# Optimization experiments

Hardware: AMD Instinct MI355X
Metric: run time of the kernel (lower is better)

Reference implementation:

```python
import jax, jax.numpy as jnp
import numpy as np

C = 1024   # n_embd = dim_att = dim_k = dim_v
H = 16     # n_head
K = 64     # k_head_size
V = 64     # v_head_size
DF = 2048  # dim_ffn = (2*C)//32*32
B = 4
T = 1024
N_LAYER = 24
LAYER_ID = 12


def setup_inputs() -> dict:
    key = jax.random.key(0)
    ks = jax.random.split(key, 8)
    r01 = LAYER_ID / (N_LAYER - 1)
    r10 = 1.0 - LAYER_ID / N_LAYER
    ddd = (jnp.arange(C, dtype=jnp.float32) / C)[None, None, :]
    maa_x = 1.0 - ddd ** r10
    maa_k = 1.0 - ddd ** r10
    maa_v = 1.0 - (ddd ** r10 + 0.3 * r01)
    maa_r = 1.0 - ddd ** (0.5 * r10)
    n = jnp.arange(C, dtype=jnp.float32)
    zigzag = ((jnp.arange(C) + 1) % 3 - 1).astype(jnp.float32) * 0.1
    u = (r01 * (1.0 - n / (C - 1)) + zigzag).reshape(H, K)
    # LoRA mats: torch init is zeros / uniform(-0.01,0.01); use small uniform for both
    # so the token-shift LoRA path is actually exercised.
    w1 = jax.random.uniform(ks[0], (C, 96), minval=-0.01, maxval=0.01)
    w2 = jax.random.uniform(ks[1], (3, 32, C), minval=-0.01, maxval=0.01)
    s = 0.02
    Wr = jax.random.normal(ks[2], (C, C)) * s
    Wk = jax.random.normal(ks[3], (C, C)) * s
    Wvg = jax.random.normal(ks[4], (C, 2 * (C + DF))) * s
    Wo = jax.random.normal(ks[5], (C + DF, C)) * s
    ln_g = jnp.ones((C,), jnp.float32)
    ln_b = jnp.zeros((C,), jnp.float32)
    x = jax.random.normal(ks[6], (B, T, C), dtype=jnp.float32)
    return dict(x=x, maa_x=maa_x, maa_k=maa_k, maa_v=maa_v, maa_r=maa_r,
                w1=w1, w2=w2, u=u, Wr=Wr, Wk=Wk, Wvg=Wvg, Wo=Wo,
                ln_g=ln_g, ln_b=ln_b)


def _wkv6(r, k, v, e, u):
    # r,k,e: (B,T,H,K); v: (B,T,H,V); u: (H,K). Decayed linear-attention scan.
    rt = r.transpose(1, 0, 2, 3)
    kt = k.transpose(1, 0, 2, 3)
    vt = v.transpose(1, 0, 2, 3)
    et = e.transpose(1, 0, 2, 3)

    def step(S, inp):  # S: (B,H,K,V)
        r_t, k_t, v_t, e_t = inp
        kv = k_t[..., :, None] * v_t[..., None, :]           # (B,H,K,V)
        out = jnp.einsum('bhk,bhkv->bhv', r_t, S + u[None, :, :, None] * kv)
        return S * e_t[..., :, None] + kv, out

    S0 = jnp.zeros((r.shape[0], u.shape[0], u.shape[1], v.shape[-1]), r.dtype)
    _, o = jax.lax.scan(step, S0, (rt, kt, vt, et))
    return o.transpose(1, 0, 2, 3)  # (B,T,H,V)


def reference(x, maa_x, maa_k, maa_v, maa_r, w1, w2, u, Wr, Wk, Wvg, Wo, ln_g, ln_b):
    Bx, Tx, Cx = x.shape
    # time_shift: ZeroPad2d((0,0,1,-1)) -> shift right by 1 along T with zero pad
    xs = jnp.concatenate([jnp.zeros_like(x[:, :1]), x[:, :-1]], axis=1)
    xx = xs - x
    xxx = x + xx * maa_x
    m = jnp.tanh(xxx @ w1).reshape(Bx, Tx, 3, -1)        # (B,T,3,32)
    m = jnp.einsum('btld,ldc->lbtc', m, w2)              # (3,B,T,C)
    mk, mv, mr = m[0], m[1], m[2]
    xk = x + xx * (maa_k + mk)
    xv = x + xx * (maa_v + mv)
    xr = x + xx * (maa_r + mr)
    r = xr @ Wr
    w = xk @ Wk
    e = jnp.exp(-jnp.exp(w))   # per-channel decay used by the WKV kernel
    k = 1.0 - e                # k = 1 - exp(-exp(w))
    vg = xv @ Wvg
    vffn, gate = jnp.split(vg, 2, axis=-1)
    vffn = vffn * jax.nn.silu(gate)
    v, ffn = vffn[..., :Cx], vffn[..., Cx:]
    o = _wkv6(r.reshape(Bx, Tx, H, K), k.reshape(Bx, Tx, H, K),
              v.reshape(Bx, Tx, H, V), e.reshape(Bx, Tx, H, K), u)
    o = o.reshape(Bx, Tx, Cx)
    mu = o.mean(-1, keepdims=True)
    var = o.var(-1, keepdims=True)
    o = (o - mu) / jnp.sqrt(var + 1e-5) * ln_g + ln_b
    return jnp.concatenate([o, ffn], axis=-1) @ Wo
```

## Files before the change

kernel.cpp:

```cpp
#include <hip/hip_runtime.h>
#include <hip/hip_bf16.h>
#include <math.h>

#define Bn 4
#define Tn 1024
#define Cn 1024
#define Hn 16
#define Kn 64
#define DFn 2048
#define NCn 16
#define Ln 64

typedef __bf16 bf16x8 __attribute__((ext_vector_type(8)));
typedef float f32x4 __attribute__((ext_vector_type(4)));

#define GLD(dst, src) \
  __builtin_amdgcn_global_load_lds((__attribute__((address_space(1))) const void*)(src), \
                                   (__attribute__((address_space(3))) void*)(dst), 16, 0, 0)

__device__ __forceinline__ float rdlane(float v, int l) {
  return __int_as_float(__builtin_amdgcn_readlane(__float_as_int(v), l));
}

__device__ __forceinline__ unsigned short bfbits(float f) {
  union { __hip_bfloat16 h; unsigned short u; } cv;
  cv.h = __float2bfloat16(f);
  return cv.u;
}

__global__ __launch_bounds__(256) void k_prep(const float* __restrict__ x,
                                              const float* __restrict__ maa_x,
                                              float* __restrict__ xx,
                                              __hip_bfloat16* __restrict__ xxx16) {
  int idx = blockIdx.x * 256 + threadIdx.x;
  int c4 = idx & 255;
  int bt = idx >> 8;
  int t = bt & (Tn - 1);
  const float4* x4 = (const float4*)x;
  float4 xv = x4[idx];
  float4 xp;
  if (t > 0) xp = x4[idx - 256];
  else { xp.x = 0.f; xp.y = 0.f; xp.z = 0.f; xp.w = 0.f; }
  float4 d;
  d.x = xp.x - xv.x; d.y = xp.y - xv.y; d.z = xp.z - xv.z; d.w = xp.w - xv.w;
  float4 m = ((const float4*)maa_x)[c4];
  ushort4 o;
  o.x = bfbits(fmaf(d.x, m.x, xv.x));
  o.y = bfbits(fmaf(d.y, m.y, xv.y));
  o.z = bfbits(fmaf(d.z, m.z, xv.z));
  o.w = bfbits(fmaf(d.w, m.w, xv.w));
  ((float4*)xx)[idx] = d;
  ((ushort4*)xxx16)[idx] = o;
}

__global__ __launch_bounds__(256) void k_mix1_16(const __hip_bfloat16* __restrict__ A,
                                                 const __hip_bfloat16* __restrict__ Bt,
                                                 __hip_bfloat16* __restrict__ m1) {
  const int K = 1024;
  __shared__ __align__(16) __hip_bfloat16 Al[128 * 32];
  __shared__ __align__(16) __hip_bfloat16 Bl[96 * 32];
  const int tid = threadIdx.x;
  const int wid = tid >> 6, lane = tid & 63;
  const int wr = wid >> 1, wc = wid & 1;
  const int row0 = blockIdx.x * 128;
  const char* gsrc[4];
  char* ldst[4];
  bool act[4];
  #pragma unroll
  for (int i = 0; i < 4; ++i) {
    const int s = i * 4 + wid;
    act[i] = (s < 14);
    const int ss = act[i] ? s : 0;
    if (ss < 8) {
      const int r = ss * 16 + (lane >> 2);
      gsrc[i] = (const char*)(A + (size_t)(row0 + r) * K) + (lane & 3) * 16;
      ldst[i] = (char*)&Al[0] + ss * 1024;
    } else {
      const int r = (ss - 8) * 16 + (lane >> 2);
      gsrc[i] = (const char*)(Bt + (size_t)r * K) + (lane & 3) * 16;
      ldst[i] = (char*)&Bl[0] + (ss - 8) * 1024;
    }
  }
  f32x4 acc[4][3];
  #pragma unroll
  for (int i = 0; i < 4; ++i)
    #pragma unroll
    for (int j = 0; j < 3; ++j)
      acc[i][j] = (f32x4){0.f, 0.f, 0.f, 0.f};
  const int g = lane >> 4, m = lane & 15;
  for (int k0 = 0; k0 < K; k0 += 32) {
    #pragma unroll
    for (int i = 0; i < 4; ++i) if (act[i]) GLD(ldst[i], gsrc[i]);
    #pragma unroll
    for (int i = 0; i < 4; ++i) gsrc[i] += 64;
    __syncthreads();
    bf16x8 af[4], bfr[3];
    #pragma unroll
    for (int i = 0; i < 4; ++i)
      af[i] = *(const bf16x8*)&Al[(wr * 64 + i * 16 + m) * 32 + g * 8];
    #pragma unroll
    for (int j = 0; j < 3; ++j)
      bfr[j] = *(const bf16x8*)&Bl[(wc * 48 + j * 16 + m) * 32 + g * 8];
    #pragma unroll
    for (int i = 0; i < 4; ++i)
      #pragma unroll
      for (int j = 0; j < 3; ++j)
        acc[i][j] = __builtin_amdgcn_mfma_f32_16x16x32_bf16(af[i], bfr[j], acc[i][j], 0, 0, 0);
    __syncthreads();
  }
  #pragma unroll
  for (int i = 0; i < 4; ++i) {
    const int grow = row0 + wr * 64 + i * 16 + g * 4;
    #pragma unroll
    for (int j = 0; j < 3; ++j) {
      const int gcol = wc * 48 + j * 16 + m;
      #pragma unroll
      for (int e = 0; e < 4; ++e)
        m1[(size_t)(grow + e) * 96 + gcol] = __float2bfloat16(tanhf(acc[i][j][e]));
    }
  }
}

__global__ __launch_bounds__(256) void k_mix2_16(const __hip_bfloat16* __restrict__ m1,
                                                 const __hip_bfloat16* __restrict__ w2t,
                                                 const float* __restrict__ x,
                                                 const float* __restrict__ xx,
                                                 const float* __restrict__ maa_k,
                                                 const float* __restrict__ maa_v,
                                                 const float* __restrict__ maa_r,
                                                 __hip_bfloat16* __restrict__ xk,
                                                 __hip_bfloat16* __restrict__ xv,
                                                 __hip_bfloat16* __restrict__ xr) {
  __shared__ __align__(16) __hip_bfloat16 Al[128 * 96];
  __shared__ __align__(16) __hip_bfloat16 Bl[3 * 64 * 32];
  const int tid = threadIdx.x;
  const int wid = tid >> 6, lane = tid & 63;
  const int wr = wid >> 1, wc = wid & 1;
  const int row0 = blockIdx.y * 128, col0 = blockIdx.x * 64;
  {
    const char* abase = (const char*)(m1 + (size_t)row0 * 96) + lane * 16;
    #pragma unroll
    for (int i = 0; i < 6; ++i) {
      const int s = wid + i * 4;
      GLD((char*)&Al[0] + s * 1024, abase + s * 1024);
    }
  }
  {
    const char* bbase = (const char*)w2t + (size_t)col0 * 64 + lane * 16;
    #pragma unroll
    for (int i = 0; i < 3; ++i) {
      const int s = wid + i * 4;
      const int l = s >> 2, q = s & 3;
      GLD((char*)&Bl[0] + s * 1024, bbase + (size_t)l * 65536 + q * 1024);
    }
  }
  __syncthreads();
  const int g = lane >> 4, m = lane & 15;
  f32x4 a0[4][2], a1[4][2], a2[4][2];
  #pragma unroll
  for (int i = 0; i < 4; ++i)
    #pragma unroll
    for (int j = 0; j < 2; ++j) {
      a0[i][j] = (f32x4){0.f,0.f,0.f,0.f};
      a1[i][j] = (f32x4){0.f,0.f,0.f,0.f};
      a2[i][j] = (f32x4){0.f,0.f,0.f,0.f};
    }
  #pragma unroll
  for (int l = 0; l < 3; ++l) {
    bf16x8 af[4], bfj[2];
    #pragma unroll
    for (int i = 0; i < 4; ++i)
      af[i] = *(const bf16x8*)&Al[(wr * 64 + i * 16 + m) * 96 + l * 32 + g * 8];
    #pragma unroll
    for (int j = 0; j < 2; ++j)
      bfj[j] = *(const bf16x8*)&Bl[(l * 64 + wc * 32 + j * 16 + m) * 32 + g * 8];
    #pragma unroll
    for (int i = 0; i < 4; ++i)
      #pragma unroll
      for (int j = 0; j < 2; ++j) {
        if (l == 0) a0[i][j] = __builtin_amdgcn_mfma_f32_16x16x32_bf16(af[i], bfj[j], a0[i][j], 0, 0, 0);
        if (l == 1) a1[i][j] = __builtin_amdgcn_mfma_f32_16x16x32_bf16(af[i], bfj[j], a1[i][j], 0, 0, 0);
        if (l == 2) a2[i][j] = __builtin_amdgcn_mfma_f32_16x16x32_bf16(af[i], bfj[j], a2[i][j], 0, 0, 0);
      }
  }
  #pragma unroll
  for (int i = 0; i < 4; ++i) {
    const int grow = row0 + wr * 64 + i * 16 + g * 4;
    #pragma unroll
    for (int j = 0; j < 2; ++j) {
      const int gcol = col0 + wc * 32 + j * 16 + m;
      const float mk_ = maa_k[gcol], mv_ = maa_v[gcol], mr_ = maa_r[gcol];
      #pragma unroll
      for (int e = 0; e < 4; ++e) {
        const size_t off = (size_t)(grow + e) * 1024 + gcol;
        const float xval = x[off], xxv = xx[off];
        xk[off] = __float2bfloat16(fmaf(xxv, mk_ + a0[i][j][e], xval));
        xv[off] = __float2bfloat16(fmaf(xxv, mv_ + a1[i][j][e], xval));
        xr[off] = __float2bfloat16(fmaf(xxv, mr_ + a2[i][j][e], xval));
      }
    }
  }
}

__global__ __launch_bounds__(256) void k_cvt_t(const float* __restrict__ W,
                                               __hip_bfloat16* __restrict__ Wt,
                                               int K, int N) {
  __shared__ float tile[32][33];
  int n0 = blockIdx.x * 32, k0 = blockIdx.y * 32;
  int tid = threadIdx.x;
  int c = tid & 31, r = tid >> 5;
  #pragma unroll
  for (int i = 0; i < 4; ++i)
    tile[r + i * 8][c] = W[(size_t)(k0 + r + i * 8) * N + n0 + c];
  __syncthreads();
  #pragma unroll
  for (int i = 0; i < 4; ++i)
    Wt[(size_t)(n0 + r + i * 8) * K + k0 + c] = __float2bfloat16(tile[c][r + i * 8]);
}

template <int FN, int EPI>
__global__ __launch_bounds__(256) void k_gemm16(const __hip_bfloat16* __restrict__ A,
                                                const __hip_bfloat16* __restrict__ Bt,
                                                float* __restrict__ C,
                                                const int K, const int N) {
  constexpr int BN = FN * 32;
  constexpr int NISS = 8 + BN / 16;
  constexpr int PW = NISS / 4;
  __shared__ __align__(16) __hip_bfloat16 Al[128 * 32];
  __shared__ __align__(16) __hip_bfloat16 Bl[BN * 32];
  const int tid = threadIdx.x;
  const int wid = tid >> 6, lane = tid & 63;
  const int wr = wid >> 1, wc = wid & 1;
  const int row0 = blockIdx.y * 128, col0 = blockIdx.x * BN;
  const char* gsrc[PW];
  char* ldst[PW];
  #pragma unroll
  for (int i = 0; i < PW; ++i) {
    const int s = wid + i * 4;
    if (s < 8) {
      const int r = s * 16 + (lane >> 2);
      gsrc[i] = (const char*)(A + (size_t)(row0 + r) * K) + (lane & 3) * 16;
      ldst[i] = (char*)&Al[0] + s * 1024;
    } else {
      const int r = (s - 8) * 16 + (lane >> 2);
      gsrc[i] = (const char*)(Bt + (size_t)(col0 + r) * K) + (lane & 3) * 16;
      ldst[i] = (char*)&Bl[0] + (s - 8) * 1024;
    }
  }
  f32x4 acc[4][FN];
  #pragma unroll
  for (int i = 0; i < 4; ++i)
    #pragma unroll
    for (int j = 0; j < FN; ++j)
      acc[i][j] = (f32x4){0.f, 0.f, 0.f, 0.f};
  const int g = lane >> 4, m = lane & 15;
  for (int k0 = 0; k0 < K; k0 += 32) {
    #pragma unroll
    for (int i = 0; i < PW; ++i) GLD(ldst[i], gsrc[i]);
    #pragma unroll
    for (int i = 0; i < PW; ++i) gsrc[i] += 64;
    __syncthreads();
    bf16x8 af[4], bfr[FN];
    #pragma unroll
    for (int i = 0; i < 4; ++i)
      af[i] = *(const bf16x8*)&Al[(wr * 64 + i * 16 + m) * 32 + g * 8];
    #pragma unroll
    for (int j = 0; j < FN; ++j)
      bfr[j] = *(const bf16x8*)&Bl[(wc * (BN / 2) + j * 16 + m) * 32 + g * 8];
    #pragma unroll
    for (int i = 0; i < 4; ++i)
      #pragma unroll
      for (int j = 0; j < FN; ++j)
        acc[i][j] = __builtin_amdgcn_mfma_f32_16x16x32_bf16(af[i], bfr[j], acc[i][j], 0, 0, 0);
    __syncthreads();
  }
  #pragma unroll
  for (int i = 0; i < 4; ++i) {
    const int grow = row0 + wr * 64 + i * 16 + g * 4;
    #pragma unroll
    for (int j = 0; j < FN; ++j) {
      const int gcol = col0 + wc * (BN / 2) + j * 16 + m;
      #pragma unroll
      for (int e = 0; e < 4; ++e) {
        float val = acc[i][j][e];
        if (EPI == 1) val = expf(-expf(val));
        C[(size_t)(grow + e) * N + gcol] = val;
      }
    }
  }
}

__global__ __launch_bounds__(256) void k_gemm_vg16(const __hip_bfloat16* __restrict__ A,
                                                   const __hip_bfloat16* __restrict__ Bt,
                                                   float* __restrict__ v,
                                                   __hip_bfloat16* __restrict__ ffn) {
  const int K = 1024;
  __shared__ __align__(16) __hip_bfloat16 Al[128 * 32];
  __shared__ __align__(16) __hip_bfloat16 B1l[64 * 32];
  __shared__ __align__(16) __hip_bfloat16 B2l[64 * 32];
  const int tid = threadIdx.x;
  const int wid = tid >> 6, lane = tid & 63;
  const int wr = wid >> 1, wc = wid & 1;
  const int row0 = blockIdx.y * 128, col0 = blockIdx.x * 64;
  const char* gsrc[4];
  char* ldst[4];
  #pragma unroll
  for (int i = 0; i < 4; ++i) {
    const int s = wid + i * 4;
    if (s < 8) {
      const int r = s * 16 + (lane >> 2);
      gsrc[i] = (const char*)(A + (size_t)(row0 + r) * K) + (lane & 3) * 16;
      ldst[i] = (char*)&Al[0] + s * 1024;
    } else if (s < 12) {
      const int r = col0 + (s - 8) * 16 + (lane >> 2);
      gsrc[i] = (const char*)(Bt + (size_t)r * K) + (lane & 3) * 16;
      ldst[i] = (char*)&B1l[0] + (s - 8) * 1024;
    } else {
      const int r = 3072 + col0 + (s - 12) * 16 + (lane >> 2);
      gsrc[i] = (const char*)(Bt + (size_t)r * K) + (lane & 3) * 16;
      ldst[i] = (char*)&B2l[0] + (s - 12) * 1024;
    }
  }
  f32x4 a1[4][2], a2[4][2];
  #pragma unroll
  for (int i = 0; i < 4; ++i)
    #pragma unroll
    for (int j = 0; j < 2; ++j) {
      a1[i][j] = (f32x4){0.f, 0.f, 0.f, 0.f};
      a2[i][j] = (f32x4){0.f, 0.f, 0.f, 0.f};
    }
  const int g = lane >> 4, m = lane & 15;
  for (int k0 = 0; k0 < K; k0 += 32) {
    #pragma unroll
    for (int i = 0; i < 4; ++i) GLD(ldst[i], gsrc[i]);
    #pragma unroll
    for (int i = 0; i < 4; ++i) gsrc[i] += 64;
    __syncthreads();
    bf16x8 af[4], b1f[2], b2f[2];
    #pragma unroll
    for (int i = 0; i < 4; ++i)
      af[i] = *(const bf16x8*)&Al[(wr * 64 + i * 16 + m) * 32 + g * 8];
    #pragma unroll
    for (int j = 0; j < 2; ++j) {
      b1f[j] = *(const bf16x8*)&B1l[(wc * 32 + j * 16 + m) * 32 + g * 8];
      b2f[j] = *(const bf16x8*)&B2l[(wc * 32 + j * 16 + m) * 32 + g * 8];
    }
    #pragma unroll
    for (int i = 0; i < 4; ++i)
      #pragma unroll
      for (int j = 0; j < 2; ++j) {
        a1[i][j] = __builtin_amdgcn_mfma_f32_16x16x32_bf16(af[i], b1f[j], a1[i][j], 0, 0, 0);
        a2[i][j] = __builtin_amdgcn_mfma_f32_16x16x32_bf16(af[i], b2f[j], a2[i][j], 0, 0, 0);
      }
    __syncthreads();
  }
  const bool to_v = (col0 < 1024);
  #pragma unroll
  for (int i = 0; i < 4; ++i) {
    const int grow = row0 + wr * 64 + i * 16 + g * 4;
    #pragma unroll
    for (int j = 0; j < 2; ++j) {
      const int gcol = col0 + wc * 32 + j * 16 + m;
      #pragma unroll
      for (int e = 0; e < 4; ++e) {
        float gate = a2[i][j][e];
        float val = a1[i][j][e] * (gate / (1.f + expf(-gate)));
        if (to_v) v[(size_t)(grow + e) * 1024 + gcol] = val;
        else ffn[(size_t)(grow + e) * 2048 + (gcol - 1024)] = __float2bfloat16(val);
      }
    }
  }
}

__global__ __launch_bounds__(256) void k_gemm_wo16(const __hip_bfloat16* __restrict__ A1,
                                                   const __hip_bfloat16* __restrict__ A2,
                                                   const __hip_bfloat16* __restrict__ Bt,
                                                   float* __restrict__ C) {
  const int Kt = 3072;
  __shared__ __align__(16) __hip_bfloat16 Al[128 * 32];
  __shared__ __align__(16) __hip_bfloat16 Bl[64 * 32];
  const int tid = threadIdx.x;
  const int wid = tid >> 6, lane = tid & 63;
  const int wr = wid >> 1, wc = wid & 1;
  const int row0 = blockIdx.y * 128, col0 = blockIdx.x * 64;
  const char* gsrc[3];
  char* ldst[3];
  #pragma unroll
  for (int i = 0; i < 3; ++i) {
    const int s = wid + i * 4;
    if (s < 8) {
      const int r = s * 16 + (lane >> 2);
      gsrc[i] = (const char*)(A1 + (size_t)(row0 + r) * 1024) + (lane & 3) * 16;
      ldst[i] = (char*)&Al[0] + s * 1024;
    } else {
      const int r = col0 + (s - 8) * 16 + (lane >> 2);
      gsrc[i] = (const char*)(Bt + (size_t)r * Kt) + (lane & 3) * 16;
      ldst[i] = (char*)&Bl[0] + (s - 8) * 1024;
    }
  }
  f32x4 acc[4][2];
  #pragma unroll
  for (int i = 0; i < 4; ++i)
    #pragma unroll
    for (int j = 0; j < 2; ++j)
      acc[i][j] = (f32x4){0.f, 0.f, 0.f, 0.f};
  const int g = lane >> 4, m = lane & 15;

  #define WO_STEP() do {                                                          \
    _Pragma("unroll")                                                             \
    for (int i = 0; i < 3; ++i) GLD(ldst[i], gsrc[i]);                            \
    _Pragma("unroll")                                                             \
    for (int i = 0; i < 3; ++i) gsrc[i] += 64;                                    \
    __syncthreads();                                                              \
    bf16x8 af[4], bfr[2];                                                         \
    _Pragma("unroll")                                                             \
    for (int i = 0; i < 4; ++i)                                                   \
      af[i] = *(const bf16x8*)&Al[(wr * 64 + i * 16 + m) * 32 + g * 8];           \
    _Pragma("unroll")                                                             \
    for (int j = 0; j < 2; ++j)                                                   \
      bfr[j] = *(const bf16x8*)&Bl[(wc * 32 + j * 16 + m) * 32 + g * 8];          \
    _Pragma("unroll")                                                             \
    for (int i = 0; i < 4; ++i)                                                   \
      _Pragma("unroll")                                                           \
      for (int j = 0; j < 2; ++j)                                                 \
        acc[i][j] = __builtin_amdgcn_mfma_f32_16x16x32_bf16(af[i], bfr[j],        \
                                                            acc[i][j], 0, 0, 0); \
    __syncthreads();                                                              \
  } while (0)

  for (int k0 = 0; k0 < 1024; k0 += 32) WO_STEP();
  #pragma unroll
  for (int i = 0; i < 3; ++i) {
    const int s = wid + i * 4;
    if (s < 8) {
      const int r = s * 16 + (lane >> 2);
      gsrc[i] = (const char*)(A2 + (size_t)(row0 + r) * 2048) + (lane & 3) * 16;
    }
  }
  for (int k0 = 0; k0 < 2048; k0 += 32) WO_STEP();
  #undef WO_STEP

  #pragma unroll
  for (int i = 0; i < 4; ++i) {
    const int grow = row0 + wr * 64 + i * 16 + g * 4;
    #pragma unroll
    for (int j = 0; j < 2; ++j) {
      const int gcol = col0 + wc * 32 + j * 16 + m;
      #pragma unroll
      for (int e = 0; e < 4; ++e)
        C[(size_t)(grow + e) * 1024 + gcol] = acc[i][j][e];
    }
  }
}

__global__ __launch_bounds__(256) void k_wkv1(const float* __restrict__ r,
                                              const float* __restrict__ e,
                                              const float* __restrict__ v,
                                              const float* __restrict__ u,
                                              float* __restrict__ o,
                                              float* __restrict__ Dcum,
                                              float* __restrict__ Dtot,
                                              float* __restrict__ Inc) {
  int blk = blockIdx.x;
  int c = blk & (NCn - 1);
  int bh = blk >> 4;
  int b = bh >> 4, h = bh & 15;
  int tid = threadIdx.x, wave = tid >> 6, lane = tid & 63;
  size_t base = (size_t)b * Tn * Cn + (size_t)h * 64 + (size_t)c * Ln * Cn;
  int jbase = wave * 16 + (lane & 15);
  float uv = u[h * 64 + jbase];
  float st[16];
  #pragma unroll
  for (int i = 0; i < 16; ++i) st[i] = 0.f;
  float cum = 1.f;
  __shared__ float yp[4][64];
  for (int t = 0; t < Ln; ++t) {
    size_t off = base + (size_t)t * Cn;
    float rv = r[off + jbase];
    float ev = e[off + jbase];
    float vv = v[off + lane];
    if (lane < 16) Dcum[off + jbase] = cum;
    cum *= ev;
    float y = 0.f;
    #pragma unroll
    for (int jj = 0; jj < 16; ++jj) {
      float rj = rdlane(rv, jj);
      float ej = rdlane(ev, jj);
      float uj = rdlane(uv, jj);
      float kv = (1.f - ej) * vv;
      y = fmaf(rj, fmaf(uj, kv, st[jj]), y);
      st[jj] = fmaf(st[jj], ej, kv);
    }
    yp[wave][lane] = y;
    __syncthreads();
    if (wave == 0)
      o[off + lane] = yp[0][lane] + yp[1][lane] + yp[2][lane] + yp[3][lane];
    __syncthreads();
  }
  size_t sbase = ((size_t)bh * NCn + c) * 4096;
  #pragma unroll
  for (int jj = 0; jj < 16; ++jj)
    Inc[sbase + (size_t)(wave * 16 + jj) * 64 + lane] = st[jj];
  if (lane < 16)
    Dtot[((size_t)bh * NCn + c) * 64 + jbase] = cum;
}

__global__ __launch_bounds__(256) void k_wkv2(float* __restrict__ S,
                                              const float* __restrict__ Dtot) {
  int bh = blockIdx.x;
  int tid = threadIdx.x;
  float4 s[4];
  #pragma unroll
  for (int j = 0; j < 4; ++j) { s[j].x = 0.f; s[j].y = 0.f; s[j].z = 0.f; s[j].w = 0.f; }
  size_t sb = (size_t)bh * NCn * 4096;
  for (int c = 0; c < NCn; ++c) {
    float4* entry = (float4*)(S + sb + (size_t)c * 4096);
    const float* dt = Dtot + ((size_t)bh * NCn + c) * 64;
    #pragma unroll
    for (int j = 0; j < 4; ++j) {
      int idx4 = tid + j * 256;
      int k = idx4 >> 4;
      float d = dt[k];
      float4 inc = entry[idx4];
      float4 cur = s[j];
      entry[idx4] = cur;
      s[j].x = fmaf(cur.x, d, inc.x);
      s[j].y = fmaf(cur.y, d, inc.y);
      s[j].z = fmaf(cur.z, d, inc.z);
      s[j].w = fmaf(cur.w, d, inc.w);
    }
  }
}

__global__ __launch_bounds__(256) void k_wkv3(const float* __restrict__ r,
                                              const float* __restrict__ Dcum,
                                              const float* __restrict__ S,
                                              float* __restrict__ o) {
  int blk = blockIdx.x;
  int c = blk & (NCn - 1);
  if (c == 0) return;
  int bh = blk >> 4;
  int b = bh >> 4, h = bh & 15;
  int tid = threadIdx.x, wave = tid >> 6, lane = tid & 63;
  const float* Sg = S + ((size_t)bh * NCn + c) * 4096;
  float sreg[64];
  #pragma unroll
  for (int k = 0; k < 64; ++k) sreg[k] = Sg[k * 64 + lane];
  size_t base = (size_t)b * Tn * Cn + (size_t)h * 64 + (size_t)c * Ln * Cn;
  for (int ti = 0; ti < 16; ++ti) {
    int t = wave * 16 + ti;
    size_t off = base + (size_t)t * Cn;
    float rd = r[off + lane] * Dcum[off + lane];
    float y = 0.f;
    #pragma unroll
    for (int k = 0; k < 64; ++k)
      y = fmaf(rdlane(rd, k), sreg[k], y);
    o[off + lane] += y;
  }
}

__global__ __launch_bounds__(256) void k_ln(const float* __restrict__ o,
                                            const float* __restrict__ g,
                                            const float* __restrict__ bta,
                                            __hip_bfloat16* __restrict__ ln16) {
  int bt = blockIdx.x, tid = threadIdx.x;
  const float4* row = (const float4*)(o + (size_t)bt * 1024);
  float4 v = row[tid];
  float s = v.x + v.y + v.z + v.w;
  float s2 = fmaf(v.x, v.x, fmaf(v.y, v.y, fmaf(v.z, v.z, v.w * v.w)));
  #pragma unroll
  for (int m = 1; m < 64; m <<= 1) {
    s += __shfl_xor(s, m, 64);
    s2 += __shfl_xor(s2, m, 64);
  }
  __shared__ float rs[4], rq[4];
  if ((tid & 63) == 0) { rs[tid >> 6] = s; rq[tid >> 6] = s2; }
  __syncthreads();
  s = rs[0] + rs[1] + rs[2] + rs[3];
  s2 = rq[0] + rq[1] + rq[2] + rq[3];
  float mu = s * (1.f / 1024.f);
  float var = s2 * (1.f / 1024.f) - mu * mu;
  float rstd = rsqrtf(var + 1e-5f);
  float4 gv = ((const float4*)g)[tid];
  float4 bv = ((const float4*)bta)[tid];
  ushort4 outv;
  outv.x = bfbits(fmaf((v.x - mu) * rstd, gv.x, bv.x));
  outv.y = bfbits(fmaf((v.y - mu) * rstd, gv.y, bv.y));
  outv.z = bfbits(fmaf((v.z - mu) * rstd, gv.z, bv.z));
  outv.w = bfbits(fmaf((v.w - mu) * rstd, gv.w, bv.w));
  ((ushort4*)((unsigned short*)ln16 + (size_t)bt * 1024))[tid] = outv;
}

extern "C" void kernel_launch(void* const* d_in, const int* in_sizes, int n_in,
                              void* d_out, int out_size, void* d_ws, size_t ws_size,
                              hipStream_t stream) {
  const float* x     = (const float*)d_in[0];
  const float* maa_x = (const float*)d_in[1];
  const float* maa_k = (const float*)d_in[2];
  const float* maa_v = (const float*)d_in[3];
  const float* maa_r = (const float*)d_in[4];
  const float* w1    = (const float*)d_in[5];
  const float* w2    = (const float*)d_in[6];
  const float* u     = (const float*)d_in[7];
  const float* Wr    = (const float*)d_in[8];
  const float* Wk    = (const float*)d_in[9];
  const float* Wvg   = (const float*)d_in[10];
  const float* Wo    = (const float*)d_in[11];
  const float* ln_g  = (const float*)d_in[12];
  const float* ln_b  = (const float*)d_in[13];
  float* out = (float*)d_out;
  float* ws = (float*)d_ws;

  const size_t M1 = 1048576;
  float* xx    = ws;
  __hip_bfloat16* xxx16 = (__hip_bfloat16*)(ws + 4 * M1);
  __hip_bfloat16* m1_16 = (__hip_bfloat16*)(ws + 8 * M1);
  __hip_bfloat16* w1t = (__hip_bfloat16*)(ws + 8 * M1 + 393216);
  __hip_bfloat16* w2t = (__hip_bfloat16*)(ws + 8 * M1 + 442368);
  __hip_bfloat16* xk16 = (__hip_bfloat16*)(ws + 8 * M1 + 524288);
  __hip_bfloat16* xv16 = (__hip_bfloat16*)(ws + 10 * M1 + 524288);
  __hip_bfloat16* xr16 = (__hip_bfloat16*)(ws + 12 * M1 + 524288);
  float* ee    = ws + 14 * M1 + 524288;
  float* vv    = ws + 18 * M1 + 524288;
  float* Sbuf  = ws + 22 * M1 + 524288;
  __hip_bfloat16* ffn16 = (__hip_bfloat16*)(ws + 26 * M1 + 524288);
  __hip_bfloat16* Wr16t = (__hip_bfloat16*)(ws + 30 * M1 + 524288);
  __hip_bfloat16* Wk16t = (__hip_bfloat16*)(ws + 31 * M1);
  __hip_bfloat16* Wvg16t = (__hip_bfloat16*)(ws + 31 * M1 + 524288);
  __hip_bfloat16* Wo16t = (__hip_bfloat16*)(ws + 34 * M1 + 524288);
  float* rr = ws + 4 * M1;
  float* oo = xx;
  float* Dcum = ws + 8 * M1 + 524288;
  float* Dtot = (float*)m1_16;
  __hip_bfloat16* ln16 = (__hip_bfloat16*)Sbuf;

  k_cvt_t<<<dim3(3, 32), 256, 0, stream>>>(w1, w1t, 1024, 96);
  k_cvt_t<<<dim3(32, 1), 256, 0, stream>>>(w2,           w2t,           32, 1024);
  k_cvt_t<<<dim3(32, 1), 256, 0, stream>>>(w2 + 32768,   w2t + 32768,   32, 1024);
  k_cvt_t<<<dim3(32, 1), 256, 0, stream>>>(w2 + 65536,   w2t + 65536,   32, 1024);
  k_cvt_t<<<dim3(32, 32), 256, 0, stream>>>(Wr, Wr16t, 1024, 1024);
  k_cvt_t<<<dim3(32, 32), 256, 0, stream>>>(Wk, Wk16t, 1024, 1024);
  k_cvt_t<<<dim3(192, 32), 256, 0, stream>>>(Wvg, Wvg16t, 1024, 6144);
  k_cvt_t<<<dim3(32, 96), 256, 0, stream>>>(Wo, Wo16t, 3072, 1024);

  k_prep<<<4096, 256, 0, stream>>>(x, maa_x, xx, xxx16);
  k_mix1_16<<<32, 256, 0, stream>>>(xxx16, w1t, m1_16);
  k_mix2_16<<<dim3(16, 32), 256, 0, stream>>>(m1_16, w2t, x, xx, maa_k, maa_v, maa_r,
                                              xk16, xv16, xr16);
  k_gemm16<2, 0><<<dim3(16, 32), 256, 0, stream>>>(xr16, Wr16t, rr, 1024, 1024);
  k_gemm_vg16<<<dim3(48, 32), 256, 0, stream>>>(xv16, Wvg16t, vv, ffn16);
  k_gemm16<2, 1><<<dim3(16, 32), 256, 0, stream>>>(xk16, Wk16t, ee, 1024, 1024);
  k_wkv1<<<64 * NCn, 256, 0, stream>>>(rr, ee, vv, u, oo, Dcum, Dtot, Sbuf);
  k_wkv2<<<64, 256, 0, stream>>>(Sbuf, Dtot);
  k_wkv3<<<64 * NCn, 256, 0, stream>>>(rr, Dcum, Sbuf, oo);
  k_ln<<<4096, 256, 0, stream>>>(oo, ln_g, ln_b, ln16);
  k_gemm_wo16<<<dim3(16, 32), 256, 0, stream>>>(ln16, ffn16, Wo16t, out);
}
```

Baseline: 360.8 us.

## Merge weight conversion launches and batch WKV chunk steps with bonus-term shuffle reduction

Folds the eight weight-transpose/convert launches into a single kernel that dispatches on block index, removing per-launch overhead. In the WKV intra-chunk kernel, loads for eight timesteps are issued at once and the cross-wave output reduction with its two barriers is done once per eight steps instead of every step. The u-bonus term is pulled out of the inner loop as a 16-lane shuffle reduction, trimming work per state element. The cost is more registers per thread and a larger shared buffer.

```diff
diff --git a/kernel.cpp b/kernel.cpp
--- a/kernel.cpp
+++ b/kernel.cpp
@@ -202,11 +202,29 @@
   }
 }
 
-__global__ __launch_bounds__(256) void k_cvt_t(const float* __restrict__ W,
-                                               __hip_bfloat16* __restrict__ Wt,
-                                               int K, int N) {
+__global__ __launch_bounds__(256) void k_cvt_all(const float* __restrict__ w1,
+                                                 const float* __restrict__ w2,
+                                                 const float* __restrict__ Wr,
+                                                 const float* __restrict__ Wk,
+                                                 const float* __restrict__ Wvg,
+                                                 const float* __restrict__ Wo,
+                                                 __hip_bfloat16* __restrict__ w1t,
+                                                 __hip_bfloat16* __restrict__ w2t,
+                                                 __hip_bfloat16* __restrict__ Wrt,
+                                                 __hip_bfloat16* __restrict__ Wkt,
+                                                 __hip_bfloat16* __restrict__ Wvgt,
+                                                 __hip_bfloat16* __restrict__ Wot) {
+  int b = blockIdx.x;
+  const float* W; __hip_bfloat16* Wt; int K, N, nx, rel;
+  if (b < 96)        { W = w1;  Wt = w1t;  K = 1024; N = 96;   nx = 3;   rel = b; }
+  else if (b < 192)  { int l = (b - 96) >> 5; rel = (b - 96) & 31;
+                       W = w2 + l * 32768; Wt = w2t + l * 32768; K = 32; N = 1024; nx = 32; }
+  else if (b < 1216) { W = Wr;  Wt = Wrt;  K = 1024; N = 1024; nx = 32;  rel = b - 192; }
+  else if (b < 2240) { W = Wk;  Wt = Wkt;  K = 1024; N = 1024; nx = 32;  rel = b - 1216; }
+  else if (b < 8384) { W = Wvg; Wt = Wvgt; K = 1024; N = 6144; nx = 192; rel = b - 2240; }
+  else               { W = Wo;  Wt = Wot;  K = 3072; N = 1024; nx = 32;  rel = b - 8384; }
+  int n0 = (rel % nx) * 32, k0 = (rel / nx) * 32;
   __shared__ float tile[32][33];
-  int n0 = blockIdx.x * 32, k0 = blockIdx.y * 32;
   int tid = threadIdx.x;
   int c = tid & 31, r = tid >> 5;
   #pragma unroll
@@ -453,6 +471,7 @@
   }
 }
 
+#define TTn 8
 __global__ __launch_bounds__(256) void k_wkv1(const float* __restrict__ r,
                                               const float* __restrict__ e,
                                               const float* __restrict__ v,
@@ -473,28 +492,48 @@
   #pragma unroll
   for (int i = 0; i < 16; ++i) st[i] = 0.f;
   float cum = 1.f;
-  __shared__ float yp[4][64];
-  for (int t = 0; t < Ln; ++t) {
-    size_t off = base + (size_t)t * Cn;
-    float rv = r[off + jbase];
-    float ev = e[off + jbase];
-    float vv = v[off + lane];
-    if (lane < 16) Dcum[off + jbase] = cum;
-    cum *= ev;
-    float y = 0.f;
-    #pragma unroll
-    for (int jj = 0; jj < 16; ++jj) {
-      float rj = rdlane(rv, jj);
-      float ej = rdlane(ev, jj);
-      float uj = rdlane(uv, jj);
-      float kv = (1.f - ej) * vv;
-      y = fmaf(rj, fmaf(uj, kv, st[jj]), y);
-      st[jj] = fmaf(st[jj], ej, kv);
-    }
-    yp[wave][lane] = y;
-    __syncthreads();
-    if (wave == 0)
-      o[off + lane] = yp[0][lane] + yp[1][lane] + yp[2][lane] + yp[3][lane];
+  __shared__ float yp[4][TTn][64];
+  for (int tb = 0; tb < Ln / TTn; ++tb) {
+    float rv8[TTn], ev8[TTn], vv8[TTn];
+    #pragma unroll
+    for (int tt = 0; tt < TTn; ++tt) {
+      size_t off = base + (size_t)(tb * TTn + tt) * Cn;
+      rv8[tt] = r[off + jbase];
+      ev8[tt] = e[off + jbase];
+      vv8[tt] = v[off + lane];
+    }
+    float yb[TTn];
+    #pragma unroll
+    for (int tt = 0; tt < TTn; ++tt) {
+      const float rv = rv8[tt], ev = ev8[tt], vv = vv8[tt];
+      if (lane < 16)
+        Dcum[base + (size_t)(tb * TTn + tt) * Cn + jbase] = cum;
+      cum *= ev;
+      float p = rv * uv * (1.f - ev);
+      p += __shfl_xor(p, 1, 16);
+      p += __shfl_xor(p, 2, 16);
+      p += __shfl_xor(p, 4, 16);
+      p += __shfl_xor(p, 8, 16);
+      float y = p * vv;
+      #pragma unroll
+      for (int jj = 0; jj < 16; ++jj) {
+        float rj = rdlane(rv, jj);
+        float ej = rdlane(ev, jj);
+        float kv = fmaf(-ej, vv, vv);
+        y = fmaf(rj, st[jj], y);
+        st[jj] = fmaf(st[jj], ej, kv);
+      }
+      yb[tt] = y;
+    }
+    #pragma unroll
+    for (int tt = 0; tt < TTn; ++tt) yp[wave][tt][lane] = yb[tt];
+    __syncthreads();
+    #pragma unroll
+    for (int q = 0; q < TTn / 4; ++q) {
+      int tt = wave * (TTn / 4) + q;
+      size_t off = base + (size_t)(tb * TTn + tt) * Cn;
+      o[off + lane] = yp[0][tt][lane] + yp[1][tt][lane] + yp[2][tt][lane] + yp[3][tt][lane];
+    }
     __syncthreads();
   }
   size_t sbase = ((size_t)bh * NCn + c) * 4096;
@@ -634,14 +673,8 @@
   float* Dtot = (float*)m1_16;
   __hip_bfloat16* ln16 = (__hip_bfloat16*)Sbuf;
 
-  k_cvt_t<<<dim3(3, 32), 256, 0, stream>>>(w1, w1t, 1024, 96);
-  k_cvt_t<<<dim3(32, 1), 256, 0, stream>>>(w2,           w2t,           32, 1024);
-  k_cvt_t<<<dim3(32, 1), 256, 0, stream>>>(w2 + 32768,   w2t + 32768,   32, 1024);
-  k_cvt_t<<<dim3(32, 1), 256, 0, stream>>>(w2 + 65536,   w2t + 65536,   32, 1024);
-  k_cvt_t<<<dim3(32, 32), 256, 0, stream>>>(Wr, Wr16t, 1024, 1024);
-  k_cvt_t<<<dim3(32, 32), 256, 0, stream>>>(Wk, Wk16t, 1024, 1024);
-  k_cvt_t<<<dim3(192, 32), 256, 0, stream>>>(Wvg, Wvg16t, 1024, 6144);
-  k_cvt_t<<<dim3(32, 96), 256, 0, stream>>>(Wo, Wo16t, 3072, 1024);
+  k_cvt_all<<<11456, 256, 0, stream>>>(w1, w2, Wr, Wk, Wvg, Wo,
+                                       w1t, w2t, Wr16t, Wk16t, Wvg16t, Wo16t);
 
   k_prep<<<4096, 256, 0, stream>>>(x, maa_x, xx, xxx16);
   k_mix1_16<<<32, 256, 0, stream>>>(xxx16, w1t, m1_16);
```

Result: faster. 339.0 us (-6.0%).
